# Performance work log

Hardware: AMD Instinct MI355X
Metric: run time of the kernel (lower is better)

Reference implementation:

```python
import jax, jax.numpy as jnp
import numpy as np
import math

RANK = 396

def setup_inputs() -> dict:
    key = jax.random.key(0)
    ks = jax.random.split(key, 8)
    batch, L, wemb, temb, tags, rank = 16, 128, 400, 20, 25, RANK
    std = 0.1545
    return {
        "word_emb": jax.random.normal(ks[0], (batch, L, wemb), dtype=jnp.float32),
        "tag_emd": jax.random.normal(ks[1], (tags, temb), dtype=jnp.float32),
        "W1": jax.random.normal(ks[2], (wemb, rank), dtype=jnp.float32) * std,
        "W2": jax.random.normal(ks[3], (wemb, rank), dtype=jnp.float32) * std,
        "W3": jax.random.normal(ks[4], (wemb, rank), dtype=jnp.float32) * std,
        "T1": jax.random.normal(ks[5], (temb, rank), dtype=jnp.float32) * std,
        "T2": jax.random.normal(ks[6], (temb, rank), dtype=jnp.float32) * std,
        "T3": jax.random.normal(ks[7], (temb, rank), dtype=jnp.float32) * std,
    }

def reference(word_emb, tag_emd, W1, W2, W3, T1, T2, T3):
    # word_emb: [n, L, wemb]; output: [n, L-2, tags, tags, tags]
    g1 = word_emb[:, :-2] @ W1   # [n, m, k]
    g2 = word_emb[:, 1:-1] @ W2
    g3 = word_emb[:, 2:] @ W3
    g4 = tag_emd @ T1            # [a, k]
    g5 = tag_emd @ T2
    g6 = tag_emd @ T3
    temp01 = g1 * g2 * g3                               # [n, m, k]
    temp02 = jnp.einsum('ak,bk,ck->abck', g4, g5, g6)   # [a, b, c, k]
    score = jnp.einsum('nmk,abck->nmabc', temp01, temp02)
    score = score / jnp.asarray(math.sqrt(RANK), score.dtype)
    return score
```

## Files before the change

kernel.cpp:

```cpp
#include <hip/hip_runtime.h>
#include <hip/hip_bf16.h>
#include <stdint.h>

#define KP    416
#define RANKD 396
#define WEMB  400
#define TEMB  20
#define TAGS  25
#define BATCH 16
#define LSEQ  128
#define MROWS 126
#define NM    2016
#define NMP   2048
#define ABC   15625
#define ABCP  15872
#define SCALE 0.050251890762960605f

typedef __attribute__((ext_vector_type(8))) short short8;
typedef __attribute__((ext_vector_type(4))) float f32x4;

#define OFF_T01  0
#define OFF_T02  1703936
#define OFF_WORD 14909440
#define OFF_WT   16613376
#define OFF_G    17651712

#define GLOAD_LDS16(gp, lp) \
  __builtin_amdgcn_global_load_lds((const __attribute__((address_space(1))) uint32_t*)(gp), \
                                   (__attribute__((address_space(3))) uint32_t*)(lp), 16, 0, 0)

__device__ __forceinline__ uint16_t f2bf(float f) {
    union { float f; uint32_t u; } v; v.f = f;
    uint32_t u = v.u;
    return (uint16_t)((u + 0x7FFFu + ((u >> 16) & 1u)) >> 16);
}

#define J1_BLK 3328
#define J2_BLK 2028
#define J3_BLK 122
__global__ void k_prep(const float* __restrict__ word,
                       const float* __restrict__ W1, const float* __restrict__ W2,
                       const float* __restrict__ W3, const float* __restrict__ tag,
                       const float* __restrict__ T1, const float* __restrict__ T2,
                       const float* __restrict__ T3,
                       uint16_t* __restrict__ wordb, uint16_t* __restrict__ wt,
                       float* __restrict__ g) {
    int bx = blockIdx.x;
    if (bx < J1_BLK) {
        int idx = bx * 256 + threadIdx.x;
        int e = idx % KP, row = idx / KP;
        wordb[idx] = f2bf((e < WEMB) ? word[row * WEMB + e] : 0.f);
    } else if (bx < J1_BLK + J2_BLK) {
        int idx = (bx - J1_BLK) * 256 + threadIdx.x;
        int j = idx / (KP * KP);
        int rem = idx % (KP * KP);
        int k = rem / KP, e = rem % KP;
        const float* W = (j == 0) ? W1 : (j == 1) ? W2 : W3;
        wt[idx] = f2bf((k < RANKD && e < WEMB) ? W[e * RANKD + k] : 0.f);
    } else {
        int idx = (bx - J1_BLK - J2_BLK) * 256 + threadIdx.x;
        if (idx >= 3 * TAGS * KP) return;
        int j = idx / (TAGS * KP);
        int rem = idx % (TAGS * KP);
        int a = rem / KP, k = rem % KP;
        const float* T = (j == 0) ? T1 : (j == 1) ? T2 : T3;
        float s = 0.f;
        if (k < RANKD) {
            for (int e = 0; e < TEMB; ++e) s += tag[a * TEMB + e] * T[e * RANKD + k];
        }
        g[idx] = s;
    }
}

#define T01_BLK 896
#define T02_BLK 3224
__global__ __launch_bounds__(256) void k_mid(const uint16_t* __restrict__ word,
                                             const uint16_t* __restrict__ wt,
                                             const float* __restrict__ g,
                                             uint16_t* __restrict__ t01,
                                             uint16_t* __restrict__ t02) {
    int bx = blockIdx.x;
    if (bx < T01_BLK) {
        int wid = threadIdx.x >> 6, lane = threadIdx.x & 63;
        int nmtile = bx & 127;
        int ktile = (bx >> 7) * 4 + wid;
        if (ktile >= KP / 16) return;
        int col_l = lane & 15, kblk = lane >> 4;
        int colk = ktile * 16 + col_l;
        f32x4 acc1 = {0.f, 0.f, 0.f, 0.f}, acc2 = acc1, acc3 = acc1;
        if (nmtile < NM / 16) {
            int nm_a = nmtile * 16 + col_l;
            int n = nm_a / MROWS, m = nm_a % MROWS;
            const uint16_t* arow = word + (size_t)(n * LSEQ + m) * KP;
            const uint16_t* b1 = wt + (size_t)colk * KP;
            const uint16_t* b2 = wt + (size_t)KP * KP + (size_t)colk * KP;
            const uint16_t* b3 = wt + (size_t)2 * KP * KP + (size_t)colk * KP;
            for (int e0 = 0; e0 < KP; e0 += 32) {
                int eo = e0 + kblk * 8;
                short8 a0 = *(const short8*)(arow + eo);
                short8 a1 = *(const short8*)(arow + KP + eo);
                short8 a2 = *(const short8*)(arow + 2 * KP + eo);
                short8 v1 = *(const short8*)(b1 + eo);
                short8 v2 = *(const short8*)(b2 + eo);
                short8 v3 = *(const short8*)(b3 + eo);
                acc1 = __builtin_amdgcn_mfma_f32_16x16x32_bf16(a0, v1, acc1, 0, 0, 0);
                acc2 = __builtin_amdgcn_mfma_f32_16x16x32_bf16(a1, v2, acc2, 0, 0, 0);
                acc3 = __builtin_amdgcn_mfma_f32_16x16x32_bf16(a2, v3, acc3, 0, 0, 0);
            }
        }
        for (int r = 0; r < 4; ++r) {
            int row = nmtile * 16 + kblk * 4 + r;
            float v = acc1[r] * acc2[r] * acc3[r] * SCALE;
            t01[(size_t)row * KP + colk] = f2bf(v);
        }
    } else {
        int idx = (bx - T01_BLK) * 256 + threadIdx.x;
        int abc = idx / (KP / 8), kc = idx % (KP / 8);
        int k0 = kc * 8;
        short8 o;
        if (abc < ABC) {
            int a = abc / 625, rem = abc % 625, b = rem / 25, c = rem % 25;
            const float4* ga = (const float4*)(g + (size_t)a * KP + k0);
            const float4* gb = (const float4*)(g + (size_t)TAGS * KP + (size_t)b * KP + k0);
            const float4* gc = (const float4*)(g + (size_t)2 * TAGS * KP + (size_t)c * KP + k0);
            float4 a0 = ga[0], a1 = ga[1];
            float4 b0 = gb[0], b1 = gb[1];
            float4 c0 = gc[0], c1 = gc[1];
            o[0] = (short)f2bf(a0.x * b0.x * c0.x);
            o[1] = (short)f2bf(a0.y * b0.y * c0.y);
            o[2] = (short)f2bf(a0.z * b0.z * c0.z);
            o[3] = (short)f2bf(a0.w * b0.w * c0.w);
            o[4] = (short)f2bf(a1.x * b1.x * c1.x);
            o[5] = (short)f2bf(a1.y * b1.y * c1.y);
            o[6] = (short)f2bf(a1.z * b1.z * c1.z);
            o[7] = (short)f2bf(a1.w * b1.w * c1.w);
        } else {
            for (int t = 0; t < 8; ++t) o[t] = 0;
        }
        *(short8*)(t02 + (size_t)abc * KP + k0) = o;
    }
}

__global__ __launch_bounds__(256, 2) void k_final(const uint16_t* __restrict__ t01,
                                                  const uint16_t* __restrict__ t02,
                                                  float* __restrict__ out) {
    __shared__ __align__(16) char smem[49152];
    float* lbuf = (float*)smem;

    const int tid = threadIdx.x;
    const int wid = tid >> 6, lane = tid & 63;
    const int col_l = lane & 15, kblk = lane >> 4;

    const int bid = blockIdx.x;
    const int swz = (bid & 7) * 124 + (bid >> 3);
    const int mb = swz & 15, nb = swz >> 4;
    const int brow = mb * 128, bcol = nb * 256;
    const int wcol = wid * 64;

    const uint16_t* gA = t01 + (size_t)(brow + (tid & 127)) * KP + (tid >> 7) * 8;
    const uint16_t* gB = t02 + (size_t)(bcol + tid) * KP;

    f32x4 acc[8][4];
#pragma unroll
    for (int m = 0; m < 8; ++m)
#pragma unroll
        for (int n = 0; n < 4; ++n)
            acc[m][n] = (f32x4){0.f, 0.f, 0.f, 0.f};

    auto stage = [&](int buf, int kt) {
        char* ab = smem + buf * 8192 + wid * 1024;
        GLOAD_LDS16(gA + kt * 32,      ab);
        GLOAD_LDS16(gA + kt * 32 + 16, ab + 4096);
        char* bb = smem + 16384 + buf * 16384 + wid * 1024;
        GLOAD_LDS16(gB + kt * 32,      bb);
        GLOAD_LDS16(gB + kt * 32 + 8,  bb + 4096);
        GLOAD_LDS16(gB + kt * 32 + 16, bb + 8192);
        GLOAD_LDS16(gB + kt * 32 + 24, bb + 12288);
    };

    const int NT = KP / 32;
    stage(0, 0);
    stage(1, 1);
    __syncthreads();

    for (int kt = 0; kt < NT; ++kt) {
        const int cur = kt & 1;
        const uint16_t* bufA = (const uint16_t*)smem + cur * 4096;
        const uint16_t* bufB = (const uint16_t*)(smem + 16384) + cur * 8192;
        short8 aF[8], bF[4];
#pragma unroll
        for (int n = 0; n < 4; ++n)
            bF[n] = *(const short8*)(bufB + kblk * 2048 + (wcol + n * 16 + col_l) * 8);
#pragma unroll
        for (int m = 0; m < 8; ++m)
            aF[m] = *(const short8*)(bufA + kblk * 1024 + (m * 16 + col_l) * 8);
#pragma unroll
        for (int m = 0; m < 8; ++m)
#pragma unroll
            for (int n = 0; n < 4; ++n)
                acc[m][n] = __builtin_amdgcn_mfma_f32_16x16x32_bf16(aF[m], bF[n], acc[m][n], 0, 0, 0);
        if (kt + 1 < NT) {
            __syncthreads();
            if (kt + 2 < NT) stage(cur, kt + 2);
        }
    }

    __syncthreads();
#pragma unroll
    for (int ch = 0; ch < 4; ++ch) {
#pragma unroll
        for (int mm = 0; mm < 2; ++mm) {
            const int m = ch * 2 + mm;
#pragma unroll
            for (int n = 0; n < 4; ++n)
#pragma unroll
                for (int r = 0; r < 4; ++r) {
                    int row_l = mm * 16 + kblk * 4 + r;
                    int col = wcol + n * 16 + col_l;
                    lbuf[row_l * 260 + col] = acc[m][n][r];
                }
        }
        __syncthreads();
#pragma unroll
        for (int r8 = 0; r8 < 8; ++r8) {
            int row_l = wid * 8 + r8;
            int grow = brow + ch * 32 + row_l;
            if (grow < NM) {
                f32x4 v = *(const f32x4*)&lbuf[row_l * 260 + lane * 4];
                int gcol = bcol + lane * 4;
                float* po = out + (size_t)grow * ABC + gcol;
                if (gcol + 3 < ABC) {
                    __builtin_nontemporal_store(v, (f32x4*)po);
                } else {
                    if (gcol     < ABC) po[0] = v[0];
                    if (gcol + 1 < ABC) po[1] = v[1];
                    if (gcol + 2 < ABC) po[2] = v[2];
                }
            }
        }
        if (ch < 3) __syncthreads();
    }
}

extern "C" void kernel_launch(void* const* d_in, const int* in_sizes, int n_in,
                              void* d_out, int out_size, void* d_ws, size_t ws_size,
                              hipStream_t stream) {
    const float* word = (const float*)d_in[0];
    const float* tag  = (const float*)d_in[1];
    const float* W1   = (const float*)d_in[2];
    const float* W2   = (const float*)d_in[3];
    const float* W3   = (const float*)d_in[4];
    const float* T1   = (const float*)d_in[5];
    const float* T2   = (const float*)d_in[6];
    const float* T3   = (const float*)d_in[7];
    float* out = (float*)d_out;
    char* ws = (char*)d_ws;

    uint16_t* t01   = (uint16_t*)(ws + OFF_T01);
    uint16_t* t02   = (uint16_t*)(ws + OFF_T02);
    uint16_t* wordb = (uint16_t*)(ws + OFF_WORD);
    uint16_t* wt    = (uint16_t*)(ws + OFF_WT);
    float*    g     = (float*)(ws + OFF_G);

    k_prep<<<J1_BLK + J2_BLK + J3_BLK, 256, 0, stream>>>(word, W1, W2, W3, tag,
                                                         T1, T2, T3, wordb, wt, g);
    k_mid<<<T01_BLK + T02_BLK, 256, 0, stream>>>(wordb, wt, g, t01, t02);
    k_final<<<16 * 62, 256, 0, stream>>>(t01, t02, out);
}
```

Measured before the change: 97.17 us.

## Shrink final GEMM tile to 128x128 with 2x2 warp layout for higher occupancy

The output GEMM block tile drops from 128x256 to 128x128, with four warps arranged 2x2 at 64x64 each. Accumulator registers and LDS use both halve, so launch bounds allow three blocks per CU. The grid roughly doubles and padding of the t02 buffer shrinks to match the new column tiling. Smaller tiles cost more A/B reloads from global memory per output element, in exchange for more blocks in flight and better wave balance on this store-bound kernel.

Result: no change. 97.37 us (+0.2%).

```diff
diff --git a/kernel.cpp b/kernel.cpp
--- a/kernel.cpp
+++ b/kernel.cpp
@@ -13,7 +13,7 @@
 #define NM    2016
 #define NMP   2048
 #define ABC   15625
-#define ABCP  15872
+#define ABCP  15744
 #define SCALE 0.050251890762960605f
 
 typedef __attribute__((ext_vector_type(8))) short short8;
@@ -21,9 +21,9 @@
 
 #define OFF_T01  0
 #define OFF_T02  1703936
-#define OFF_WORD 14909440
-#define OFF_WT   16613376
-#define OFF_G    17651712
+#define OFF_WORD 14802944
+#define OFF_WT   16506880
+#define OFF_G    17545216
 
 #define GLOAD_LDS16(gp, lp) \
   __builtin_amdgcn_global_load_lds((const __attribute__((address_space(1))) uint32_t*)(gp), \
@@ -73,7 +73,7 @@
 }
 
 #define T01_BLK 896
-#define T02_BLK 3224
+#define T02_BLK 3198
 __global__ __launch_bounds__(256) void k_mid(const uint16_t* __restrict__ word,
                                              const uint16_t* __restrict__ wt,
                                              const float* __restrict__ g,
@@ -141,10 +141,10 @@
     }
 }
 
-__global__ __launch_bounds__(256, 2) void k_final(const uint16_t* __restrict__ t01,
+__global__ __launch_bounds__(256, 3) void k_final(const uint16_t* __restrict__ t01,
                                                   const uint16_t* __restrict__ t02,
                                                   float* __restrict__ out) {
-    __shared__ __align__(16) char smem[49152];
+    __shared__ __align__(16) char smem[32768];
     float* lbuf = (float*)smem;
 
     const int tid = threadIdx.x;
@@ -152,30 +152,29 @@
     const int col_l = lane & 15, kblk = lane >> 4;
 
     const int bid = blockIdx.x;
-    const int swz = (bid & 7) * 124 + (bid >> 3);
+    const int swz = (bid & 7) * 246 + (bid >> 3);
     const int mb = swz & 15, nb = swz >> 4;
-    const int brow = mb * 128, bcol = nb * 256;
-    const int wcol = wid * 64;
-
-    const uint16_t* gA = t01 + (size_t)(brow + (tid & 127)) * KP + (tid >> 7) * 8;
-    const uint16_t* gB = t02 + (size_t)(bcol + tid) * KP;
-
-    f32x4 acc[8][4];
-#pragma unroll
-    for (int m = 0; m < 8; ++m)
+    const int brow = mb * 128, bcol = nb * 128;
+
+    const int wrow = (wid >> 1) * 64, wcol = (wid & 1) * 64;
+
+    const int rS = (wid & 1) * 64 + lane, ksS = wid >> 1;
+    const uint16_t* gA = t01 + (size_t)(brow + rS) * KP + ksS * 8;
+    const uint16_t* gB = t02 + (size_t)(bcol + rS) * KP + ksS * 8;
+
+    f32x4 acc[4][4];
+#pragma unroll
+    for (int m = 0; m < 4; ++m)
 #pragma unroll
         for (int n = 0; n < 4; ++n)
             acc[m][n] = (f32x4){0.f, 0.f, 0.f, 0.f};
 
     auto stage = [&](int buf, int kt) {
-        char* ab = smem + buf * 8192 + wid * 1024;
-        GLOAD_LDS16(gA + kt * 32,      ab);
-        GLOAD_LDS16(gA + kt * 32 + 16, ab + 4096);
-        char* bb = smem + 16384 + buf * 16384 + wid * 1024;
-        GLOAD_LDS16(gB + kt * 32,      bb);
-        GLOAD_LDS16(gB + kt * 32 + 8,  bb + 4096);
-        GLOAD_LDS16(gB + kt * 32 + 16, bb + 8192);
-        GLOAD_LDS16(gB + kt * 32 + 24, bb + 12288);
+        char* base = smem + buf * 16384;
+        GLOAD_LDS16(gA + kt * 32,      base + wid * 1024);
+        GLOAD_LDS16(gA + kt * 32 + 16, base + 4096 + wid * 1024);
+        GLOAD_LDS16(gB + kt * 32,      base + 8192 + wid * 1024);
+        GLOAD_LDS16(gB + kt * 32 + 16, base + 8192 + 4096 + wid * 1024);
     };
 
     const int NT = KP / 32;
@@ -185,17 +184,17 @@
 
     for (int kt = 0; kt < NT; ++kt) {
         const int cur = kt & 1;
-        const uint16_t* bufA = (const uint16_t*)smem + cur * 4096;
-        const uint16_t* bufB = (const uint16_t*)(smem + 16384) + cur * 8192;
-        short8 aF[8], bF[4];
+        const uint16_t* bufA = (const uint16_t*)(smem + cur * 16384);
+        const uint16_t* bufB = bufA + 4096;
+        short8 aF[4], bF[4];
 #pragma unroll
         for (int n = 0; n < 4; ++n)
-            bF[n] = *(const short8*)(bufB + kblk * 2048 + (wcol + n * 16 + col_l) * 8);
-#pragma unroll
-        for (int m = 0; m < 8; ++m)
-            aF[m] = *(const short8*)(bufA + kblk * 1024 + (m * 16 + col_l) * 8);
-#pragma unroll
-        for (int m = 0; m < 8; ++m)
+            bF[n] = *(const short8*)(bufB + kblk * 1024 + (wcol + n * 16 + col_l) * 8);
+#pragma unroll
+        for (int m = 0; m < 4; ++m)
+            aF[m] = *(const short8*)(bufA + kblk * 1024 + (wrow + m * 16 + col_l) * 8);
+#pragma unroll
+        for (int m = 0; m < 4; ++m)
 #pragma unroll
             for (int n = 0; n < 4; ++n)
                 acc[m][n] = __builtin_amdgcn_mfma_f32_16x16x32_bf16(aF[m], bF[n], acc[m][n], 0, 0, 0);
@@ -208,26 +207,28 @@
     __syncthreads();
 #pragma unroll
     for (int ch = 0; ch < 4; ++ch) {
-#pragma unroll
-        for (int mm = 0; mm < 2; ++mm) {
-            const int m = ch * 2 + mm;
-#pragma unroll
-            for (int n = 0; n < 4; ++n)
-#pragma unroll
-                for (int r = 0; r < 4; ++r) {
-                    int row_l = mm * 16 + kblk * 4 + r;
-                    int col = wcol + n * 16 + col_l;
-                    lbuf[row_l * 260 + col] = acc[m][n][r];
-                }
+        if ((wid >> 1) == (ch >> 1)) {
+#pragma unroll
+            for (int mm = 0; mm < 2; ++mm) {
+                const int m = (ch & 1) * 2 + mm;
+#pragma unroll
+                for (int n = 0; n < 4; ++n)
+#pragma unroll
+                    for (int r = 0; r < 4; ++r) {
+                        int row_l = mm * 16 + kblk * 4 + r;
+                        int col = wcol + n * 16 + col_l;
+                        lbuf[row_l * 132 + col] = acc[m][n][r];
+                    }
+            }
         }
         __syncthreads();
 #pragma unroll
-        for (int r8 = 0; r8 < 8; ++r8) {
-            int row_l = wid * 8 + r8;
+        for (int it = 0; it < 4; ++it) {
+            int row_l = it * 8 + (tid >> 5);
             int grow = brow + ch * 32 + row_l;
+            int gcol = bcol + (tid & 31) * 4;
             if (grow < NM) {
-                f32x4 v = *(const f32x4*)&lbuf[row_l * 260 + lane * 4];
-                int gcol = bcol + lane * 4;
+                f32x4 v = *(const f32x4*)&lbuf[row_l * 132 + (tid & 31) * 4];
                 float* po = out + (size_t)grow * ABC + gcol;
                 if (gcol + 3 < ABC) {
                     __builtin_nontemporal_store(v, (f32x4*)po);
@@ -265,5 +266,5 @@
     k_prep<<<J1_BLK + J2_BLK + J3_BLK, 256, 0, stream>>>(word, W1, W2, W3, tag,
                                                          T1, T2, T3, wordb, wt, g);
     k_mid<<<T01_BLK + T02_BLK, 256, 0, stream>>>(wordb, wt, g, t01, t02);
-    k_final<<<16 * 62, 256, 0, stream>>>(t01, t02, out);
-}
+    k_final<<<16 * 123, 256, 0, stream>>>(t01, t02, out);
+}
```

## Shrink final GEMM tile to 64 rows, keep A in LDS, stream B via registers

Applied to the files above, without the earlier changes.

The final GEMM tile drops from 128x256 to 64x256 rows and the grid doubles. The whole 64xK A tile is loaded into LDS once up front, while each wave reads its B fragments straight from global memory into registers, prefetching one k-step ahead. This removes the per-k-step __syncthreads and the LDS double buffering, and lowers register pressure by halving the accumulators. The cost is less reuse of B across rows, so t02 is read twice as often, and B loads are not coalesced through LDS.

After: 82.53 us. 15.1% less time.

```diff
diff --git a/kernel.cpp b/kernel.cpp
--- a/kernel.cpp
+++ b/kernel.cpp
@@ -141,73 +141,72 @@
     }
 }
 
-__global__ __launch_bounds__(256, 2) void k_final(const uint16_t* __restrict__ t01,
-                                                  const uint16_t* __restrict__ t02,
-                                                  float* __restrict__ out) {
-    __shared__ __align__(16) char smem[49152];
-    float* lbuf = (float*)smem;
+__global__ __launch_bounds__(256) void k_final(const uint16_t* __restrict__ t01,
+                                               const uint16_t* __restrict__ t02,
+                                               float* __restrict__ out) {
+    __shared__ __align__(16) uint16_t ldsA[64 * KP];
+    float* lbuf = (float*)ldsA;
 
     const int tid = threadIdx.x;
     const int wid = tid >> 6, lane = tid & 63;
     const int col_l = lane & 15, kblk = lane >> 4;
 
-    const int bid = blockIdx.x;
-    const int swz = (bid & 7) * 124 + (bid >> 3);
-    const int mb = swz & 15, nb = swz >> 4;
-    const int brow = mb * 128, bcol = nb * 256;
+    const int gidx = (blockIdx.x & 7) * 248 + (blockIdx.x >> 3);
+    const int mb = gidx & 31, nb = gidx >> 5;
+    const int brow = mb * 64, bcol = nb * 256;
     const int wcol = wid * 64;
 
-    const uint16_t* gA = t01 + (size_t)(brow + (tid & 127)) * KP + (tid >> 7) * 8;
-    const uint16_t* gB = t02 + (size_t)(bcol + tid) * KP;
-
-    f32x4 acc[8][4];
-#pragma unroll
-    for (int m = 0; m < 8; ++m)
+    {
+        const uint16_t* gAsrc = t01 + (size_t)(brow + lane) * KP + wid * 8;
+        char* ldst = (char*)ldsA + wid * 1024;
+#pragma unroll
+        for (int t = 0; t < 13; ++t)
+            GLOAD_LDS16(gAsrc + t * 32, ldst + t * 4096);
+    }
+
+    const uint16_t* gBn[4];
+#pragma unroll
+    for (int n = 0; n < 4; ++n)
+        gBn[n] = t02 + (size_t)(bcol + wcol + n * 16 + col_l) * KP + kblk * 8;
+
+    f32x4 acc[4][4];
+#pragma unroll
+    for (int m = 0; m < 4; ++m)
 #pragma unroll
         for (int n = 0; n < 4; ++n)
             acc[m][n] = (f32x4){0.f, 0.f, 0.f, 0.f};
 
-    auto stage = [&](int buf, int kt) {
-        char* ab = smem + buf * 8192 + wid * 1024;
-        GLOAD_LDS16(gA + kt * 32,      ab);
-        GLOAD_LDS16(gA + kt * 32 + 16, ab + 4096);
-        char* bb = smem + 16384 + buf * 16384 + wid * 1024;
-        GLOAD_LDS16(gB + kt * 32,      bb);
-        GLOAD_LDS16(gB + kt * 32 + 8,  bb + 4096);
-        GLOAD_LDS16(gB + kt * 32 + 16, bb + 8192);
-        GLOAD_LDS16(gB + kt * 32 + 24, bb + 12288);
-    };
+    short8 bP[4];
+#pragma unroll
+    for (int n = 0; n < 4; ++n) bP[n] = *(const short8*)(gBn[n]);
+
+    __syncthreads();
 
     const int NT = KP / 32;
-    stage(0, 0);
-    stage(1, 1);
-    __syncthreads();
-
+#pragma unroll
     for (int kt = 0; kt < NT; ++kt) {
-        const int cur = kt & 1;
-        const uint16_t* bufA = (const uint16_t*)smem + cur * 4096;
-        const uint16_t* bufB = (const uint16_t*)(smem + 16384) + cur * 8192;
-        short8 aF[8], bF[4];
-#pragma unroll
-        for (int n = 0; n < 4; ++n)
-            bF[n] = *(const short8*)(bufB + kblk * 2048 + (wcol + n * 16 + col_l) * 8);
-#pragma unroll
-        for (int m = 0; m < 8; ++m)
-            aF[m] = *(const short8*)(bufA + kblk * 1024 + (m * 16 + col_l) * 8);
-#pragma unroll
-        for (int m = 0; m < 8; ++m)
+        short8 bF[4];
+#pragma unroll
+        for (int n = 0; n < 4; ++n) bF[n] = bP[n];
+        if (kt + 1 < NT) {
+#pragma unroll
+            for (int n = 0; n < 4; ++n)
+                bP[n] = *(const short8*)(gBn[n] + (kt + 1) * 32);
+        }
+        short8 aF[4];
+#pragma unroll
+        for (int m = 0; m < 4; ++m)
+            aF[m] = *(const short8*)(ldsA + (kt * 4 + kblk) * 512 + (m * 16 + col_l) * 8);
+#pragma unroll
+        for (int m = 0; m < 4; ++m)
 #pragma unroll
             for (int n = 0; n < 4; ++n)
                 acc[m][n] = __builtin_amdgcn_mfma_f32_16x16x32_bf16(aF[m], bF[n], acc[m][n], 0, 0, 0);
-        if (kt + 1 < NT) {
-            __syncthreads();
-            if (kt + 2 < NT) stage(cur, kt + 2);
-        }
     }
 
     __syncthreads();
 #pragma unroll
-    for (int ch = 0; ch < 4; ++ch) {
+    for (int ch = 0; ch < 2; ++ch) {
 #pragma unroll
         for (int mm = 0; mm < 2; ++mm) {
             const int m = ch * 2 + mm;
@@ -222,12 +221,12 @@
         }
         __syncthreads();
 #pragma unroll
-        for (int r8 = 0; r8 < 8; ++r8) {
-            int row_l = wid * 8 + r8;
+        for (int it = 0; it < 8; ++it) {
+            int row_l = it * 4 + wid;
             int grow = brow + ch * 32 + row_l;
+            int gcol = bcol + lane * 4;
             if (grow < NM) {
                 f32x4 v = *(const f32x4*)&lbuf[row_l * 260 + lane * 4];
-                int gcol = bcol + lane * 4;
                 float* po = out + (size_t)grow * ABC + gcol;
                 if (gcol + 3 < ABC) {
                     __builtin_nontemporal_store(v, (f32x4*)po);
@@ -238,7 +237,7 @@
                 }
             }
         }
-        if (ch < 3) __syncthreads();
+        if (ch == 0) __syncthreads();
     }
 }
 
@@ -265,5 +264,5 @@
     k_prep<<<J1_BLK + J2_BLK + J3_BLK, 256, 0, stream>>>(word, W1, W2, W3, tag,
                                                          T1, T2, T3, wordb, wt, g);
     k_mid<<<T01_BLK + T02_BLK, 256, 0, stream>>>(wordb, wt, g, t01, t02);
-    k_final<<<16 * 62, 256, 0, stream>>>(t01, t02, out);
-}
+    k_final<<<32 * 62, 256, 0, stream>>>(t01, t02, out);
+}
```
